# Kernel tuning notes

Measured on AMD Instinct MI355X. Metric: run time of the kernel, lower is better.

The kernel has to match this reference:

```python
import jax, jax.numpy as jnp
import numpy as np
import math

N = 50000   # nodes
E = 800000  # edges
D = 128     # in/out dim
T = 4       # node types
H = 8       # heads (forced: Linear(8,64).view(-1, H, 8))
DK = D // H
HD = 8      # h_mat feature dim


def setup_inputs() -> dict:
    key = jax.random.key(0)
    ks = jax.random.split(key, 16)
    g = lambda k, shp, fan: jax.random.uniform(k, shp, jnp.float32, -1.0, 1.0) * math.sqrt(6.0 / fan)
    return {
        "meta_xs": jax.random.normal(ks[0], (N, D), jnp.float32),
        "node_type": jax.random.randint(ks[1], (N,), 0, T),
        "edge_index": jax.random.randint(ks[2], (2, E), 0, N),
        "h_mat": jax.random.normal(ks[3], (N, HD), jnp.float32),
        "sub_W": g(ks[4], (T, D, D), 2 * D),
        "sub_b": jnp.zeros((T, D), jnp.float32),
        "neigh_W": g(ks[5], (T, D, D), 2 * D),
        "neigh_b": jnp.zeros((T, D), jnp.float32),
        "hsub_W": g(ks[6], (HD, H * HD), HD + H * HD),
        "hsub_b": jnp.zeros((H * HD,), jnp.float32),
        "hneigh_W": g(ks[7], (HD, H * HD), HD + H * HD),
        "hneigh_b": jnp.zeros((H * HD,), jnp.float32),
        "relation_att": g(ks[8], (T, H, DK), H + DK),
        "relation_h_att": g(ks[9], (T, H, HD), H + HD),
        "ln_gamma": jnp.ones((D,), jnp.float32),
        "ln_beta": jnp.zeros((D,), jnp.float32),
    }


def _hgt_forward(meta_xs, h_mat, sub_W, sub_b, neigh_W, neigh_b, hsub_W, hsub_b,
                 hneigh_W, hneigh_b, relation_att, relation_h_att, ln_gamma, ln_beta,
                 node_type, edge_index):
    n = meta_xs.shape[0]
    e = edge_index.shape[1]
    src = edge_index[0]  # edge_index_j (neighbor)
    dst = edge_index[1]  # edge_index_i (sub / target)
    sqrt_dk = math.sqrt(DK)
    d_h = math.sqrt(H)

    # per-node, type-selected linear projections (sub by own type, neigh by own type)
    q_all = jnp.einsum('nd,tdo->tno', meta_xs, sub_W) + sub_b[:, None, :]      # [T,N,D]
    k_all = jnp.einsum('nd,tdo->tno', meta_xs, neigh_W) + neigh_b[:, None, :]  # [T,N,D]
    ar = jnp.arange(n)
    q_node = q_all[node_type, ar]  # [N,D] sub_linear[type_i](x_i)
    k_node = k_all[node_type, ar]  # [N,D] neigh_linear[type_j](x_j)

    h_sub_node = (h_mat @ hsub_W + hsub_b).reshape(n, H, HD)
    h_neigh_node = (h_mat @ hneigh_W + hneigh_b).reshape(n, H, HD)

    st = node_type[dst]  # sub type per edge selects relation params
    h_s = h_sub_node[dst]    # [E,H,8]
    h_n = h_neigh_node[src]  # [E,H,8]
    att_h = jnp.sum(jnp.tanh(h_s * h_n) * relation_h_att[st], axis=-1) / d_h  # [E,H]

    q_e = q_node[dst].reshape(e, H, DK)
    k_e = k_node[src].reshape(e, H, DK)
    att = jnp.sum(jnp.tanh(q_e * k_e) * relation_att[st], axis=-1) / sqrt_dk * att_h  # [E,H]

    # edge softmax over destination segments
    m = jax.ops.segment_max(att, dst, num_segments=n)  # [N,H]
    ea = jnp.exp(att - m[dst])
    denom = jax.ops.segment_sum(ea, dst, num_segments=n)
    alpha = ea / (denom[dst] + 1e-16)  # [E,H]

    msg = (k_e * alpha[:, :, None]).reshape(e, D)
    aggr = jax.ops.segment_sum(msg, dst, num_segments=n)  # [N,D]

    out = jax.nn.gelu(aggr, approximate=False)
    mu = jnp.mean(out, axis=-1, keepdims=True)
    var = jnp.var(out, axis=-1, keepdims=True)
    return (out - mu) * jax.lax.rsqrt(var + 1e-5) * ln_gamma + ln_beta


def reference(meta_xs, node_type, edge_index, h_mat, sub_W, sub_b, neigh_W, neigh_b,
              hsub_W, hsub_b, hneigh_W, hneigh_b, relation_att, relation_h_att,
              ln_gamma, ln_beta):
    return _hgt_forward(meta_xs, h_mat, sub_W, sub_b, neigh_W, neigh_b, hsub_W, hsub_b,
                        hneigh_W, hneigh_b, relation_att, relation_h_att, ln_gamma, ln_beta,
                        node_type, edge_index)
```

## Files before the change

### kernel.cpp

```cpp
#include <hip/hip_runtime.h>

typedef __bf16 bf16x8 __attribute__((ext_vector_type(8)));
typedef float f32x4 __attribute__((ext_vector_type(4)));

__device__ __forceinline__ float exp2_fast(float x){
#if __has_builtin(__builtin_amdgcn_exp2f)
  return __builtin_amdgcn_exp2f(x);
#else
  return __expf(x * 0.69314718055994531f);
#endif
}
template<int CTRL>
__device__ __forceinline__ float dpp_add(float x){
  union { float f; int i; } a, b;
  a.f = x;
  b.i = __builtin_amdgcn_mov_dpp(a.i, CTRL, 0xF, 0xF, true);
  return x + b.f;
}
__device__ __forceinline__ float sum4(float x){
  x = dpp_add<0xB1>(x);
  x = dpp_add<0x4E>(x);
  return x;
}
__device__ __forceinline__ unsigned int cvt_pk_bf16(float lo, float hi){
  unsigned int r;
  asm("v_cvt_pk_bf16_f32 %0, %1, %2" : "=v"(r) : "v"(lo), "v"(hi));
  return r;
}
__device__ __forceinline__ unsigned short f2bf1(float f){
  return (unsigned short)cvt_pk_bf16(f, f);
}
__device__ __forceinline__ bf16x8 ld_bf8(const unsigned short* p){
  union { uint4 u; bf16x8 v; } c;
  c.u = *reinterpret_cast<const uint4*>(p);
  return c.v;
}
__device__ __forceinline__ bf16x8 ld_f32_to_bf8(const float* p){
  float4 lo = *reinterpret_cast<const float4*>(p);
  float4 hi = *reinterpret_cast<const float4*>(p + 4);
  union { unsigned int u[4]; bf16x8 v; } c;
  c.u[0] = cvt_pk_bf16(lo.x, lo.y);
  c.u[1] = cvt_pk_bf16(lo.z, lo.w);
  c.u[2] = cvt_pk_bf16(hi.x, hi.y);
  c.u[3] = cvt_pk_bf16(hi.z, hi.w);
  return c.v;
}

__global__ __launch_bounds__(1024) void k_types(const int* ntype, int* tmeta, int N){
  __shared__ int cnt[4];
  int tid = threadIdx.x;
  if (tid < 4) cnt[tid] = 0;
  __syncthreads();
  int c0=0,c1=0,c2=0,c3=0;
  for (int i = tid; i < N; i += 1024){
    int t = ntype[i];
    c0 += (t==0); c1 += (t==1); c2 += (t==2); c3 += (t==3);
  }
  if (c0) atomicAdd(&cnt[0], c0);
  if (c1) atomicAdd(&cnt[1], c1);
  if (c2) atomicAdd(&cnt[2], c2);
  if (c3) atomicAdd(&cnt[3], c3);
  __syncthreads();
  if (tid == 0){
    int a = 0;
    tmeta[4] = 0;
    for (int k = 0; k < 4; ++k){ tmeta[k] = cnt[k]; a += cnt[k]; tmeta[5+k] = a; }
    for (int k = 0; k < 4; ++k) tmeta[9+k] = tmeta[4+k];
  }
}

__global__ void k_init_nbt(const int* ntype, int* cursor, int* tcur, int* nbt, int N){
  int i = blockIdx.x*blockDim.x + threadIdx.x;
  if (i >= N) return;
  cursor[i << 4] = 0;
  int lane = threadIdx.x & 63;
  int myt = ntype[i];
  unsigned long long below = (lane == 0) ? 0ull : ((~0ull) >> (64 - lane));
  #pragma unroll
  for (int tt = 0; tt < 4; ++tt){
    unsigned long long mask = __ballot(myt == tt);
    if (mask){
      int leader = __ffsll((long long)mask) - 1;
      int base = 0;
      if (lane == leader) base = atomicAdd(&tcur[tt], __popcll(mask));
      base = __shfl(base, leader);
      if (myt == tt){
        int pos = base + __popcll(mask & below);
        nbt[pos] = i;
      }
    }
  }
}

__global__ void k_ll_h_w(const int* ei, int* cursor, unsigned short* bucket, int E,
                         const float* h_mat, const float* hsW, const float* hsb,
                         const float* hnW, const float* hnb,
                         float2* hs2, char* khc, int N, int HB, int LB,
                         const float* subW, const float* neighW,
                         unsigned short* wts, unsigned short* wtn){
  int b = blockIdx.x;
  if (b < HB){
    int i = b*256 + threadIdx.x;
    if (i >= N*32) return;
    int n = i >> 5, l = i & 31;
    const float* hm = h_mat + (size_t)n*8;
    const float2* hsW2 = reinterpret_cast<const float2*>(hsW);
    const float2* hnW2 = reinterpret_cast<const float2*>(hnW);
    float s0=0.f, s1=0.f, n0=0.f, n1=0.f;
    #pragma unroll
    for (int d = 0; d < 8; ++d){
      float hv = hm[d];
      float2 ws2 = hsW2[d*32 + l];
      float2 wn2 = hnW2[d*32 + l];
      s0 += hv * ws2.x; s1 += hv * ws2.y;
      n0 += hv * wn2.x; n1 += hv * wn2.y;
    }
    float2 bs = reinterpret_cast<const float2*>(hsb)[l];
    float2 bn = reinterpret_cast<const float2*>(hnb)[l];
    hs2[(size_t)i] = make_float2(s0 + bs.x, s1 + bs.y);
    *reinterpret_cast<unsigned int*>(khc + (size_t)n*512 + l*16 + 8)
        = cvt_pk_bf16(n0 + bn.x, n1 + bn.y);
  } else if (b < HB + LB){
    int i = (b - HB)*256 + threadIdx.x;
    if (i >= E) return;
    int d = ei[E + i];
    int s = ei[i];
    int pos = atomicAdd(&cursor[d << 4], 1);
    if (pos < 128) bucket[(size_t)d*128 + pos] = (unsigned short)s;
  } else {
    int i = (b - HB - LB)*256 + threadIdx.x;
    int w = i >> 16;
    int r = i & 65535;
    int t = r >> 14;
    int rem = r & 16383;
    int o = rem >> 7;
    int kd = rem & 127;
    const float* src = w ? neighW : subW;
    unsigned short* dstp = w ? wtn : wts;
    dstp[(t << 14) + (o << 7) + kd] = f2bf1(src[(t << 14) + (kd << 7) + o]);
  }
}

__global__ __launch_bounds__(256) void k_qk_mfma(const float* X,
      const unsigned short* wts, const unsigned short* wtn,
      const float* sub_b, const float* neigh_b,
      const int* nbt, const int* toff,
      float* q, char* khc){
  int b = blockIdx.x;
  int t = -1, chunk = 0, acc = 0;
  #pragma unroll
  for (int tt = 0; tt < 4; ++tt){
    int cnt = toff[tt+1] - toff[tt];
    int nc = (cnt + 63) >> 6;
    if (t < 0 && b < acc + nc){ t = tt; chunk = b - acc; }
    acc += nc;
  }
  if (t < 0) return;
  int lane = threadIdx.x & 63;
  int w = threadIdx.x >> 6;
  int quad = lane >> 4, l16 = lane & 15;
  int base = toff[t] + chunk*64 + w*16;
  int endp = toff[t+1];
  int p = base + l16;
  int nid = nbt[p < endp ? p : toff[t]];
  bf16x8 a[4];
  #pragma unroll
  for (int kk = 0; kk < 4; ++kk)
    a[kk] = ld_f32_to_bf8(X + (size_t)nid*128 + kk*32 + quad*8);
  int nidr[4]; bool okr[4];
  #pragma unroll
  for (int reg = 0; reg < 4; ++reg){
    int pr = base + quad*4 + reg;
    okr[reg] = pr < endp;
    nidr[reg] = nbt[pr < endp ? pr : toff[t]];
  }
  #pragma unroll
  for (int pj = 0; pj < 2; ++pj){
    const unsigned short* Wt = pj ? wtn : wts;
    const float* bias = pj ? neigh_b : sub_b;
    #pragma unroll
    for (int ot = 0; ot < 8; ++ot){
      int o = ot*16 + l16;
      f32x4 c = {0.f, 0.f, 0.f, 0.f};
      #pragma unroll
      for (int kk = 0; kk < 4; ++kk){
        bf16x8 bfr = ld_bf8(Wt + ((size_t)t << 14) + ((size_t)o << 7) + kk*32 + quad*8);
        c = __builtin_amdgcn_mfma_f32_16x16x32_bf16(a[kk], bfr, c, 0, 0, 0);
      }
      float bv = bias[t*128 + o];
      #pragma unroll
      for (int reg = 0; reg < 4; ++reg){
        if (okr[reg]){
          float v = c[reg] + bv;
          if (pj == 0){
            q[(size_t)nidr[reg]*128 + o] = v;
          } else {
            size_t off = ((size_t)nidr[reg] << 9)
                       + (size_t)(((o >> 2) << 4) + (((o >> 1) & 1) << 2) + ((o & 1) << 1));
            *reinterpret_cast<unsigned short*>(khc + off) = f2bf1(v);
          }
        }
      }
    }
  }
}

__global__ __launch_bounds__(256) void k_edge(const float* q, const char* khc,
      const float2* hs2, const int* cursor, const unsigned short* bucket,
      const int* ntype,
      const float* rel_att, const float* rel_h_att,
      const float* ln_g, const float* ln_b,
      float* out, int N){
  int wid = (blockIdx.x*blockDim.x + threadIdx.x) >> 6;
  if (wid >= N) return;
  int lane = threadIdx.x & 63;
  int l = lane & 31;
  int half = (lane >> 5) & 1;
  int t4 = l & 3, head = l >> 2;
  const float TLOG2E = 2.8853900817779268f;
  float4 qv = *reinterpret_cast<const float4*>(q + (size_t)wid*128 + l*4);
  float qe0 = qv.x*TLOG2E, qe1 = qv.y*TLOG2E, qe2 = qv.z*TLOG2E, qe3 = qv.w*TLOG2E;
  float2 hv = hs2[(size_t)wid*32 + l];
  float he0 = hv.x*TLOG2E, he1 = hv.y*TLOG2E;
  int st = ntype[wid];
  int rb = st*8 + head;
  float4 ra = *reinterpret_cast<const float4*>(rel_att + rb*16 + t4*4);
  float2 rh = *reinterpret_cast<const float2*>(rel_h_att + rb*8 + t4*2);
  float c0 = -0.5f*ra.x, c1 = -0.5f*ra.y, c2 = -0.5f*ra.z, c3 = -0.5f*ra.w;
  float cs = 0.25f*(ra.x + ra.y + ra.z + ra.w);
  const float HSC = 0.35355339059327373f * 1.4426950408889634f;
  float rh0 = rh.x*HSC, rh1 = rh.y*HSC;
  float ch0 = -2.f*rh0, ch1 = -2.f*rh1, chs = rh0 + rh1;
  float s = 0.f, a0 = 0.f, a1 = 0.f, a2 = 0.f, a3 = 0.f;

  int deg = __builtin_amdgcn_readfirstlane(cursor[wid << 4]);
  if (deg > 128) deg = 128;
  unsigned bkt = reinterpret_cast<const unsigned*>(bucket)[(size_t)wid*64 + lane];
  int niter = (deg + 1) >> 1;
  const char* kh_l = khc + l*16;

  auto lp = [&](int g)->uint4 {
    int gg = g < niter ? g : 0;
    unsigned v = (unsigned)__builtin_amdgcn_readlane((int)bkt, gg);
    int sA = (int)(v & 0xffffu);
    int sB = (2*gg + 1 < deg) ? (int)(v >> 16) : sA;
    int sy = half ? sB : sA;
    return *reinterpret_cast<const uint4*>(kh_l + ((size_t)(unsigned)sy << 9));
  };
  auto pr = [&](uint4 P, int g){
    union { unsigned u; float f; } k0,k1,k2,k3,h0,h1;
    k0.u = P.x << 16; k1.u = P.x & 0xffff0000u;
    k2.u = P.y << 16; k3.u = P.y & 0xffff0000u;
    h0.u = P.z << 16; h1.u = P.z & 0xffff0000u;
    float e0 = exp2_fast(qe0*k0.f), e1 = exp2_fast(qe1*k1.f);
    float e2 = exp2_fast(qe2*k2.f), e3 = exp2_fast(qe3*k3.f);
    float f0 = exp2_fast(he0*h0.f), f1 = exp2_fast(he1*h1.f);
    float r0 = __builtin_amdgcn_rcpf(e0 + 1.f), r1 = __builtin_amdgcn_rcpf(e1 + 1.f);
    float r2 = __builtin_amdgcn_rcpf(e2 + 1.f), r3 = __builtin_amdgcn_rcpf(e3 + 1.f);
    float g0 = __builtin_amdgcn_rcpf(f0 + 1.f), g1 = __builtin_amdgcn_rcpf(f1 + 1.f);
    float pp = fmaf(c0,r0, fmaf(c1,r1, fmaf(c2,r2, fmaf(c3,r3, cs))));
    float ph = fmaf(ch0,g0, fmaf(ch1,g1, chs));
    pp = sum4(pp);
    ph = sum4(ph);
    float w = exp2_fast(pp * ph);
    w = (2*g + half < deg) ? w : 0.f;
    s += w;
    a0 = fmaf(w, k0.f, a0); a1 = fmaf(w, k1.f, a1);
    a2 = fmaf(w, k2.f, a2); a3 = fmaf(w, k3.f, a3);
  };

  if (niter > 0){
    uint4 A = lp(0);
    uint4 B = lp(1);
    for (int g = 0; g < niter; g += 2){
      uint4 C = lp(g+2);
      pr(A, g);
      uint4 D = lp(g+3);
      if (g+1 < niter) pr(B, g+1);
      A = C; B = D;
    }
  }
  s  += __shfl_xor(s, 32);
  a0 += __shfl_xor(a0, 32); a1 += __shfl_xor(a1, 32);
  a2 += __shfl_xor(a2, 32); a3 += __shfl_xor(a3, 32);

  float inv = 1.0f / (s + 1e-16f);
  float x0 = a0*inv, x1 = a1*inv, x2 = a2*inv, x3 = a3*inv;
  const float IS2 = 0.70710678118654752f;
  x0 = 0.5f*x0*(1.f + erff(x0*IS2));
  x1 = 0.5f*x1*(1.f + erff(x1*IS2));
  x2 = 0.5f*x2*(1.f + erff(x2*IS2));
  x3 = 0.5f*x3*(1.f + erff(x3*IS2));
  float sm = x0+x1+x2+x3;
  float sq = x0*x0 + x1*x1 + x2*x2 + x3*x3;
  #pragma unroll
  for (int d = 1; d < 32; d <<= 1){ sm += __shfl_xor(sm, d); sq += __shfl_xor(sq, d); }
  float mu = sm * (1.f/128.f);
  float var = fmaxf(sq * (1.f/128.f) - mu*mu, 0.f);
  float r = rsqrtf(var + 1e-5f);
  if (half == 0){
    float4 g4 = *reinterpret_cast<const float4*>(ln_g + l*4);
    float4 b4 = *reinterpret_cast<const float4*>(ln_b + l*4);
    float4 o4 = make_float4((x0-mu)*r*g4.x + b4.x, (x1-mu)*r*g4.y + b4.y,
                            (x2-mu)*r*g4.z + b4.z, (x3-mu)*r*g4.w + b4.w);
    *reinterpret_cast<float4*>(out + (size_t)wid*128 + l*4) = o4;
  }
}

extern "C" void kernel_launch(void* const* d_in, const int* in_sizes, int n_in,
                              void* d_out, int out_size, void* d_ws, size_t ws_size,
                              hipStream_t stream) {
  const float* meta_xs  = (const float*)d_in[0];
  const int*   node_type= (const int*)d_in[1];
  const int*   edge_idx = (const int*)d_in[2];
  const float* h_mat    = (const float*)d_in[3];
  const float* sub_W    = (const float*)d_in[4];
  const float* sub_b    = (const float*)d_in[5];
  const float* neigh_W  = (const float*)d_in[6];
  const float* neigh_b  = (const float*)d_in[7];
  const float* hsub_W   = (const float*)d_in[8];
  const float* hsub_b   = (const float*)d_in[9];
  const float* hneigh_W = (const float*)d_in[10];
  const float* hneigh_b = (const float*)d_in[11];
  const float* rel_att  = (const float*)d_in[12];
  const float* rel_hatt = (const float*)d_in[13];
  const float* ln_g     = (const float*)d_in[14];
  const float* ln_b     = (const float*)d_in[15];

  const int N = in_sizes[0] / 128;
  const int E = in_sizes[2] / 2;

  char* wbase = (char*)d_ws;
  size_t o = 0;
  auto carve = [&](size_t bytes)->char* {
    char* p = wbase + o;
    o = (o + bytes + 255) & ~(size_t)255;
    return p;
  };
  float*          q      = (float*)carve((size_t)N*128*4);
  char*           kh2    = carve((size_t)N*512);
  float2*         hs2    = (float2*)carve((size_t)N*32*8);
  unsigned short* bucket = (unsigned short*)carve((size_t)N*128*2);
  int*            cursor = (int*)carve((size_t)N*16*4);
  int*            nbt    = (int*)carve((size_t)N*4);
  int*            tmeta  = (int*)carve(64);
  unsigned short* wts    = (unsigned short*)carve((size_t)4*128*128*2);
  unsigned short* wtn    = (unsigned short*)carve((size_t)4*128*128*2);
  if (o > ws_size) return;

  int* toff = tmeta + 4;
  int* tcur = tmeta + 9;

  const int HB = (N*32 + 255) / 256;
  const int LB = (E + 255) / 256;
  const int WB = (2*4*128*128) / 256;

  k_types   <<<1, 1024, 0, stream>>>(node_type, tmeta, N);
  k_init_nbt<<<(N+255)/256, 256, 0, stream>>>(node_type, cursor, tcur, nbt, N);
  k_ll_h_w  <<<HB + LB + WB, 256, 0, stream>>>(edge_idx, cursor, bucket, E,
                                               h_mat, hsub_W, hsub_b, hneigh_W, hneigh_b,
                                               hs2, kh2, N, HB, LB,
                                               sub_W, neigh_W, wts, wtn);
  k_qk_mfma <<<((N+63)>>6)+4, 256, 0, stream>>>(meta_xs, wts, wtn, sub_b, neigh_b,
                                                nbt, toff, q, kh2);
  k_edge    <<<(N+3)/4, 256, 0, stream>>>(q, kh2, hs2, cursor, bucket, node_type,
                                          rel_att, rel_hatt, ln_g, ln_b,
                                          (float*)d_out, N);
}
```

Measured before the change: 329.4 us.

## Fold type bucketing into setup kernel, split K/H storage, vectorize QK stores

Drops the separate type-count and node-bucketing kernels. A memset now clears the cursors and type counters, and nodes are bucketed into padded per-type arrays inside the fused setup kernel, which removes two launches and a serial single-block pass. The interleaved 512-byte K+H record is split into a dense bf16 K array and a separate bf16 h_neigh array. The MFMA operands are swapped so each lane writes contiguous float4/uint2 outputs instead of scattered scalars. The edge kernel now issues two gathers per edge (8 bytes and 4 bytes) instead of one 16-byte load, which may add memory transactions on the hot gather path.

Result: faster. 290.4 us (-11.9%).

```diff
diff --git a/kernel.cpp b/kernel.cpp
--- a/kernel.cpp
+++ b/kernel.cpp
@@ -46,61 +46,43 @@
   return c.v;
 }
 
-__global__ __launch_bounds__(1024) void k_types(const int* ntype, int* tmeta, int N){
-  __shared__ int cnt[4];
-  int tid = threadIdx.x;
-  if (tid < 4) cnt[tid] = 0;
-  __syncthreads();
-  int c0=0,c1=0,c2=0,c3=0;
-  for (int i = tid; i < N; i += 1024){
-    int t = ntype[i];
-    c0 += (t==0); c1 += (t==1); c2 += (t==2); c3 += (t==3);
-  }
-  if (c0) atomicAdd(&cnt[0], c0);
-  if (c1) atomicAdd(&cnt[1], c1);
-  if (c2) atomicAdd(&cnt[2], c2);
-  if (c3) atomicAdd(&cnt[3], c3);
-  __syncthreads();
-  if (tid == 0){
-    int a = 0;
-    tmeta[4] = 0;
-    for (int k = 0; k < 4; ++k){ tmeta[k] = cnt[k]; a += cnt[k]; tmeta[5+k] = a; }
-    for (int k = 0; k < 4; ++k) tmeta[9+k] = tmeta[4+k];
-  }
-}
-
-__global__ void k_init_nbt(const int* ntype, int* cursor, int* tcur, int* nbt, int N){
-  int i = blockIdx.x*blockDim.x + threadIdx.x;
-  if (i >= N) return;
-  cursor[i << 4] = 0;
-  int lane = threadIdx.x & 63;
-  int myt = ntype[i];
-  unsigned long long below = (lane == 0) ? 0ull : ((~0ull) >> (64 - lane));
-  #pragma unroll
-  for (int tt = 0; tt < 4; ++tt){
-    unsigned long long mask = __ballot(myt == tt);
-    if (mask){
-      int leader = __ffsll((long long)mask) - 1;
-      int base = 0;
-      if (lane == leader) base = atomicAdd(&tcur[tt], __popcll(mask));
-      base = __shfl(base, leader);
-      if (myt == tt){
-        int pos = base + __popcll(mask & below);
-        nbt[pos] = i;
-      }
-    }
-  }
-}
-
 __global__ void k_ll_h_w(const int* ei, int* cursor, unsigned short* bucket, int E,
+                         const int* ntype, int* tcur, int* nbt, int Npad, int N,
                          const float* h_mat, const float* hsW, const float* hsb,
                          const float* hnW, const float* hnb,
-                         float2* hs2, char* khc, int N, int HB, int LB,
+                         float2* hs2, char* hnc, int LB, int NB, int HB,
                          const float* subW, const float* neighW,
                          unsigned short* wts, unsigned short* wtn){
   int b = blockIdx.x;
-  if (b < HB){
+  if (b < LB){
     int i = b*256 + threadIdx.x;
+    if (i >= E) return;
+    int d = ei[E + i];
+    int s = ei[i];
+    int pos = atomicAdd(&cursor[d << 4], 1);
+    if (pos < 128) bucket[(size_t)d*128 + pos] = (unsigned short)s;
+  } else if (b < LB + NB){
+    int i = (b - LB)*256 + threadIdx.x;
+    if (i >= N) return;
+    int lane = threadIdx.x & 63;
+    int myt = ntype[i];
+    unsigned long long below = (lane == 0) ? 0ull : ((~0ull) >> (64 - lane));
+    #pragma unroll
+    for (int tt = 0; tt < 4; ++tt){
+      unsigned long long mask = __ballot(myt == tt);
+      if (mask){
+        int leader = __ffsll((long long)mask) - 1;
+        int base = 0;
+        if (lane == leader) base = atomicAdd(&tcur[tt], __popcll(mask));
+        base = __shfl(base, leader);
+        if (myt == tt){
+          int pos = base + __popcll(mask & below);
+          nbt[tt*Npad + pos] = i;
+        }
+      }
+    }
+  } else if (b < LB + NB + HB){
+    int i = (b - LB - NB)*256 + threadIdx.x;
     if (i >= N*32) return;
     int n = i >> 5, l = i & 31;
     const float* hm = h_mat + (size_t)n*8;
@@ -118,17 +100,10 @@
     float2 bs = reinterpret_cast<const float2*>(hsb)[l];
     float2 bn = reinterpret_cast<const float2*>(hnb)[l];
     hs2[(size_t)i] = make_float2(s0 + bs.x, s1 + bs.y);
-    *reinterpret_cast<unsigned int*>(khc + (size_t)n*512 + l*16 + 8)
+    *reinterpret_cast<unsigned int*>(hnc + (size_t)n*128 + l*4)
         = cvt_pk_bf16(n0 + bn.x, n1 + bn.y);
-  } else if (b < HB + LB){
-    int i = (b - HB)*256 + threadIdx.x;
-    if (i >= E) return;
-    int d = ei[E + i];
-    int s = ei[i];
-    int pos = atomicAdd(&cursor[d << 4], 1);
-    if (pos < 128) bucket[(size_t)d*128 + pos] = (unsigned short)s;
   } else {
-    int i = (b - HB - LB)*256 + threadIdx.x;
+    int i = (b - LB - NB - HB)*256 + threadIdx.x;
     int w = i >> 16;
     int r = i & 65535;
     int t = r >> 14;
@@ -144,13 +119,13 @@
 __global__ __launch_bounds__(256) void k_qk_mfma(const float* X,
       const unsigned short* wts, const unsigned short* wtn,
       const float* sub_b, const float* neigh_b,
-      const int* nbt, const int* toff,
-      float* q, char* khc){
+      const int* nbt, const int* tcur, int Npad,
+      float* q, char* kkc){
   int b = blockIdx.x;
   int t = -1, chunk = 0, acc = 0;
   #pragma unroll
   for (int tt = 0; tt < 4; ++tt){
-    int cnt = toff[tt+1] - toff[tt];
+    int cnt = tcur[tt];
     int nc = (cnt + 63) >> 6;
     if (t < 0 && b < acc + nc){ t = tt; chunk = b - acc; }
     acc += nc;
@@ -159,55 +134,47 @@
   int lane = threadIdx.x & 63;
   int w = threadIdx.x >> 6;
   int quad = lane >> 4, l16 = lane & 15;
-  int base = toff[t] + chunk*64 + w*16;
-  int endp = toff[t+1];
-  int p = base + l16;
-  int nid = nbt[p < endp ? p : toff[t]];
-  bf16x8 a[4];
+  int cnt = tcur[t];
+  int p = chunk*64 + w*16 + l16;
+  bool ok = p < cnt;
+  int nid = nbt[t*Npad + (ok ? p : 0)];
+  bf16x8 xb[4];
   #pragma unroll
   for (int kk = 0; kk < 4; ++kk)
-    a[kk] = ld_f32_to_bf8(X + (size_t)nid*128 + kk*32 + quad*8);
-  int nidr[4]; bool okr[4];
-  #pragma unroll
-  for (int reg = 0; reg < 4; ++reg){
-    int pr = base + quad*4 + reg;
-    okr[reg] = pr < endp;
-    nidr[reg] = nbt[pr < endp ? pr : toff[t]];
-  }
+    xb[kk] = ld_f32_to_bf8(X + (size_t)nid*128 + kk*32 + quad*8);
   #pragma unroll
   for (int pj = 0; pj < 2; ++pj){
     const unsigned short* Wt = pj ? wtn : wts;
     const float* bias = pj ? neigh_b : sub_b;
     #pragma unroll
     for (int ot = 0; ot < 8; ++ot){
-      int o = ot*16 + l16;
       f32x4 c = {0.f, 0.f, 0.f, 0.f};
       #pragma unroll
       for (int kk = 0; kk < 4; ++kk){
-        bf16x8 bfr = ld_bf8(Wt + ((size_t)t << 14) + ((size_t)o << 7) + kk*32 + quad*8);
-        c = __builtin_amdgcn_mfma_f32_16x16x32_bf16(a[kk], bfr, c, 0, 0, 0);
+        bf16x8 wa = ld_bf8(Wt + ((size_t)t << 14) + ((size_t)(ot*16 + l16) << 7)
+                              + kk*32 + quad*8);
+        c = __builtin_amdgcn_mfma_f32_16x16x32_bf16(wa, xb[kk], c, 0, 0, 0);
       }
-      float bv = bias[t*128 + o];
-      #pragma unroll
-      for (int reg = 0; reg < 4; ++reg){
-        if (okr[reg]){
-          float v = c[reg] + bv;
-          if (pj == 0){
-            q[(size_t)nidr[reg]*128 + o] = v;
-          } else {
-            size_t off = ((size_t)nidr[reg] << 9)
-                       + (size_t)(((o >> 2) << 4) + (((o >> 1) & 1) << 2) + ((o & 1) << 1));
-            *reinterpret_cast<unsigned short*>(khc + off) = f2bf1(v);
-          }
+      int o0 = ot*16 + quad*4;
+      float4 b4 = *reinterpret_cast<const float4*>(bias + t*128 + o0);
+      if (ok){
+        if (pj == 0){
+          float4 v = make_float4(c[0]+b4.x, c[1]+b4.y, c[2]+b4.z, c[3]+b4.w);
+          *reinterpret_cast<float4*>(q + (size_t)nid*128 + o0) = v;
+        } else {
+          uint2 pk;
+          pk.x = cvt_pk_bf16(c[0]+b4.x, c[1]+b4.y);
+          pk.y = cvt_pk_bf16(c[2]+b4.z, c[3]+b4.w);
+          *reinterpret_cast<uint2*>(kkc + ((size_t)nid << 8) + (size_t)(o0 << 1)) = pk;
         }
       }
     }
   }
 }
 
-__global__ __launch_bounds__(256) void k_edge(const float* q, const char* khc,
-      const float2* hs2, const int* cursor, const unsigned short* bucket,
-      const int* ntype,
+__global__ __launch_bounds__(256) void k_edge(const float* q, const char* kkc,
+      const char* hnc, const float2* hs2, const int* cursor,
+      const unsigned short* bucket, const int* ntype,
       const float* rel_att, const float* rel_h_att,
       const float* ln_g, const float* ln_b,
       float* out, int N){
@@ -237,21 +204,26 @@
   if (deg > 128) deg = 128;
   unsigned bkt = reinterpret_cast<const unsigned*>(bucket)[(size_t)wid*64 + lane];
   int niter = (deg + 1) >> 1;
-  const char* kh_l = khc + l*16;
-
-  auto lp = [&](int g)->uint4 {
+  const char* kk_l = kkc + l*8;
+  const char* hn_l = hnc + l*4;
+
+  struct KH { uint2 k; unsigned h; };
+  auto lp = [&](int g)->KH {
     int gg = g < niter ? g : 0;
     unsigned v = (unsigned)__builtin_amdgcn_readlane((int)bkt, gg);
     int sA = (int)(v & 0xffffu);
     int sB = (2*gg + 1 < deg) ? (int)(v >> 16) : sA;
     int sy = half ? sB : sA;
-    return *reinterpret_cast<const uint4*>(kh_l + ((size_t)(unsigned)sy << 9));
+    KH r;
+    r.k = *reinterpret_cast<const uint2*>(kk_l + ((size_t)(unsigned)sy << 8));
+    r.h = *reinterpret_cast<const unsigned*>(hn_l + ((size_t)(unsigned)sy << 7));
+    return r;
   };
-  auto pr = [&](uint4 P, int g){
+  auto pr = [&](KH P, int g){
     union { unsigned u; float f; } k0,k1,k2,k3,h0,h1;
-    k0.u = P.x << 16; k1.u = P.x & 0xffff0000u;
-    k2.u = P.y << 16; k3.u = P.y & 0xffff0000u;
-    h0.u = P.z << 16; h1.u = P.z & 0xffff0000u;
+    k0.u = P.k.x << 16; k1.u = P.k.x & 0xffff0000u;
+    k2.u = P.k.y << 16; k3.u = P.k.y & 0xffff0000u;
+    h0.u = P.h << 16;   h1.u = P.h & 0xffff0000u;
     float e0 = exp2_fast(qe0*k0.f), e1 = exp2_fast(qe1*k1.f);
     float e2 = exp2_fast(qe2*k2.f), e3 = exp2_fast(qe3*k3.f);
     float f0 = exp2_fast(he0*h0.f), f1 = exp2_fast(he1*h1.f);
@@ -270,12 +242,12 @@
   };
 
   if (niter > 0){
-    uint4 A = lp(0);
-    uint4 B = lp(1);
+    KH A = lp(0);
+    KH B = lp(1);
     for (int g = 0; g < niter; g += 2){
-      uint4 C = lp(g+2);
+      KH C = lp(g+2);
       pr(A, g);
-      uint4 D = lp(g+3);
+      KH D = lp(g+3);
       if (g+1 < niter) pr(B, g+1);
       A = C; B = D;
     }
@@ -329,6 +301,7 @@
 
   const int N = in_sizes[0] / 128;
   const int E = in_sizes[2] / 2;
+  const int Npad = (N + 63) & ~63;
 
   char* wbase = (char*)d_ws;
   size_t o = 0;
@@ -338,32 +311,33 @@
     return p;
   };
   float*          q      = (float*)carve((size_t)N*128*4);
-  char*           kh2    = carve((size_t)N*512);
+  char*           kkc    = carve((size_t)N*256);
+  char*           hnc    = carve((size_t)N*128);
   float2*         hs2    = (float2*)carve((size_t)N*32*8);
   unsigned short* bucket = (unsigned short*)carve((size_t)N*128*2);
   int*            cursor = (int*)carve((size_t)N*16*4);
-  int*            nbt    = (int*)carve((size_t)N*4);
   int*            tmeta  = (int*)carve(64);
+  int*            nbt    = (int*)carve((size_t)4*Npad*4);
   unsigned short* wts    = (unsigned short*)carve((size_t)4*128*128*2);
   unsigned short* wtn    = (unsigned short*)carve((size_t)4*128*128*2);
   if (o > ws_size) return;
 
-  int* toff = tmeta + 4;
-  int* tcur = tmeta + 9;
-
+  int* tcur = tmeta;
+
+  const int LB = (E + 255) / 256;
+  const int NB = (N + 255) / 256;
   const int HB = (N*32 + 255) / 256;
-  const int LB = (E + 255) / 256;
   const int WB = (2*4*128*128) / 256;
 
-  k_types   <<<1, 1024, 0, stream>>>(node_type, tmeta, N);
-  k_init_nbt<<<(N+255)/256, 256, 0, stream>>>(node_type, cursor, tcur, nbt, N);
-  k_ll_h_w  <<<HB + LB + WB, 256, 0, stream>>>(edge_idx, cursor, bucket, E,
+  hipMemsetAsync(cursor, 0, (size_t)N*64 + 64, stream);
+  k_ll_h_w  <<<LB + NB + HB + WB, 256, 0, stream>>>(edge_idx, cursor, bucket, E,
+                                               node_type, tcur, nbt, Npad, N,
                                                h_mat, hsub_W, hsub_b, hneigh_W, hneigh_b,
-                                               hs2, kh2, N, HB, LB,
+                                               hs2, hnc, LB, NB, HB,
                                                sub_W, neigh_W, wts, wtn);
   k_qk_mfma <<<((N+63)>>6)+4, 256, 0, stream>>>(meta_xs, wts, wtn, sub_b, neigh_b,
-                                                nbt, toff, q, kh2);
-  k_edge    <<<(N+3)/4, 256, 0, stream>>>(q, kh2, hs2, cursor, bucket, node_type,
+                                                nbt, tcur, Npad, q, kkc);
+  k_edge    <<<(N+3)/4, 256, 0, stream>>>(q, kkc, hnc, hs2, cursor, bucket, node_type,
                                           rel_att, rel_hatt, ln_g, ln_b,
                                           (float*)d_out, N);
 }
```
